# Performance work log

Measured on AMD Instinct MI355X. Metric: run time of the kernel, lower is better.

## Reference

```python
import jax, jax.numpy as jnp
import numpy as np

B, N0, N1, FD, L, H = 4, 256, 256, 128, 3, 1
NG = N0 + N1            # nodes per graph
N = B * NG              # total nodes
EPS_BN = 1e-5
EPS_SM = 1e-16


def _build_edges():
    def perm_edges(n, off):
        idx = np.arange(n)
        a = np.repeat(idx, n); b = np.tile(idx, n)
        m = a != b
        return np.stack([a[m], b[m]]) + off
    e_intra = np.concatenate([perm_edges(N0, 0), perm_edges(N1, N0)], axis=1)
    a = np.arange(N0); b = np.arange(N0, N0 + N1)
    cross1 = np.stack([np.repeat(a, N1), np.tile(b, N0)])
    cross2 = np.stack([np.repeat(b, N0), np.tile(a, N1)])
    eg = np.concatenate([e_intra, cross1, cross2], axis=1)
    tg = np.concatenate([np.zeros(e_intra.shape[1], np.int32),
                         np.ones(cross1.shape[1] + cross2.shape[1], np.int32)])
    ei = np.concatenate([eg + g * NG for g in range(B)], axis=1).astype(np.int32)
    et = np.tile(tg, B).astype(np.int32)
    return jnp.asarray(ei), jnp.asarray(et)


def setup_inputs() -> dict:
    key = jax.random.key(0)
    ks = jax.random.split(key, 8)
    edge_index, edge_type = _build_edges()
    return {
        'desc0': jax.random.normal(ks[0], (B, FD, N0), jnp.float32),
        'desc1': jax.random.normal(ks[1], (B, FD, N1), jnp.float32),
        'W': jax.random.normal(ks[2], (L, 2, FD, H * FD), jnp.float32) * (1.0 / np.sqrt(FD)),
        'q': jax.random.normal(ks[3], (L, H * FD, H), jnp.float32) * 0.1,
        'k': jax.random.normal(ks[4], (L, H * FD, H), jnp.float32) * 0.1,
        'conv_b': jnp.zeros((L, FD), jnp.float32),
        'lin_W': jax.random.normal(ks[5], (L, FD, 2 * FD), jnp.float32) * (1.0 / np.sqrt(2 * FD)),
        'lin_b': jnp.zeros((L, FD), jnp.float32),
        'gamma': jnp.ones((L, FD), jnp.float32),
        'beta': jnp.zeros((L, FD), jnp.float32),
        'edge_index': edge_index,
        'edge_type': edge_type,
    }


def _forward(desc0, desc1, W, q, k, conv_b, lin_W, lin_b, gamma, beta, edge_index, edge_type):
    # x: [B, NG, FD] -> flattened batch graph [N, FD]
    x = jnp.concatenate([desc0, desc1], axis=2)        # [B, FD, NG]
    x = jnp.transpose(x, (0, 2, 1)).reshape(N, FD)
    src, dst = edge_index[0], edge_index[1]
    nlayers = W.shape[0]
    heads = q.shape[2]
    for l in range(nlayers):
        # relation-specific node projections (equiv to per-edge bmm with weight[edge_type])
        proj = jnp.einsum('nf,rfo->nro', x, W[l])       # [N, 2, H*FD]
        out_i = proj[dst, edge_type]                    # [E, H*FD]
        out_j = proj[src, edge_type]                    # [E, H*FD]
        alpha = jax.nn.leaky_relu(out_i @ q[l] + out_j @ k[l], 0.2)  # [E, H]
        # softmax over incoming edges of each destination node (across-relation)
        amax = jax.ops.segment_max(alpha, dst, num_segments=N)
        ex = jnp.exp(alpha - amax[dst])
        denom = jax.ops.segment_sum(ex, dst, num_segments=N)
        att = ex / (denom[dst] + EPS_SM)                # [E, H]
        msg = (att[:, :, None] * out_j.reshape(-1, heads, FD)).reshape(-1, heads * FD)
        agg = jax.ops.segment_sum(msg, dst, num_segments=N).reshape(N, heads, FD)
        m1 = jax.nn.relu(agg.mean(axis=1) + conv_b[l])  # concat=False -> mean over heads
        m2 = jnp.concatenate([x, m1], axis=1) @ lin_W[l].T + lin_b[l]
        mu = m2.mean(axis=0)
        var = ((m2 - mu) ** 2).mean(axis=0)             # biased var (BatchNorm training)
        m3 = (m2 - mu) / jnp.sqrt(var + EPS_BN) * gamma[l] + beta[l]
        x = x + m3
    x = x.reshape(B, NG, FD).transpose(0, 2, 1)         # [B, FD, NG]
    return x


def reference(desc0, desc1, W, q, k, conv_b, lin_W, lin_b, gamma, beta, edge_index, edge_type):
    x = _forward(desc0, desc1, W, q, k, conv_b, lin_W, lin_b, gamma, beta, edge_index, edge_type)
    return x[:, :, :N0], x[:, :, N0:]
```

## Files before the change

### kernel.cpp

```cpp
#include <hip/hip_runtime.h>

#define FD  128
#define NN  2048

#define OFF_X     0
#define OFF_PROJ  262144
#define OFF_QS    786432
#define OFF_KS    790528
#define OFF_SUMS  794624
#define OFF_LWT   800768
#define OFF_M2    899072

__device__ __forceinline__ int swizzle_n0(int bid) {
    int g    = (bid & 7) >> 1;
    int slot = ((bid >> 3) << 1) | (bid & 1);
    return g*512 + slot*4;
}

__device__ __forceinline__ void proj_qsks4(
    const float* __restrict__ W, const float* __restrict__ qv,
    const float* __restrict__ kv, float* __restrict__ ws,
    int l, int n0, int t, const float (*xs)[FD],
    float (*redp)[256], float* red)
{
    int kh = t >> 8, tp = t & 255;
    int rsel = tp >> 7, o = tp & 127;
    const float* Wl = W + ((size_t)(l*2 + rsel)*FD)*FD + o;
    float acc[4];
#pragma unroll
    for (int r = 0; r < 4; r++) acc[r] = 0.f;
    int kbase = kh * 64;
#pragma unroll
    for (int kk = 0; kk < 64; kk += 4) {
        int k4 = kbase + kk;
        float w0 = Wl[(k4+0)*FD], w1 = Wl[(k4+1)*FD];
        float w2 = Wl[(k4+2)*FD], w3 = Wl[(k4+3)*FD];
#pragma unroll
        for (int r = 0; r < 4; r++) {
            float4 xq = *(const float4*)&xs[r][k4];
            acc[r] += xq.x*w0 + xq.y*w1 + xq.z*w2 + xq.w*w3;
        }
    }
    if (kh == 1) {
#pragma unroll
        for (int r = 0; r < 4; r++) redp[r][tp] = acc[r];
    }
    __syncthreads();
    if (t < 256) {
#pragma unroll
        for (int r = 0; r < 4; r++) acc[r] += redp[r][tp];
#pragma unroll
        for (int r = 0; r < 4; r++)
            ws[OFF_PROJ + (size_t)(n0 + r)*256 + tp] = acc[r];

        float qq = qv[l*FD + o], kq = kv[l*FD + o];
        int lane = t & 63, w = t >> 6;
#pragma unroll
        for (int r = 0; r < 4; r++) {
            float vq = acc[r]*qq, vk = acc[r]*kq;
            for (int off = 32; off; off >>= 1) {
                vq += __shfl_xor(vq, off, 64);
                vk += __shfl_xor(vk, off, 64);
            }
            if (lane == 0) { red[w*8 + r*2] = vq; red[w*8 + r*2 + 1] = vk; }
        }
    }
    __syncthreads();
    if (t < 16) {
        int r = t & 3, rs = (t >> 2) & 1, wh = t >> 3;
        float v = red[(rs*2)*8 + r*2 + wh] + red[(rs*2 + 1)*8 + r*2 + wh];
        if (wh == 0) ws[OFF_QS + rs*NN + n0 + r] = v;
        else         ws[OFF_KS + rs*NN + n0 + r] = v;
    }
}

__global__ __launch_bounds__(512, 4) void k_pre(
    const float* __restrict__ d0, const float* __restrict__ d1,
    const float* __restrict__ W,  const float* __restrict__ qv,
    const float* __restrict__ kv, const float* __restrict__ linW,
    float* __restrict__ ws)
{
    int bid = blockIdx.x, t = threadIdx.x;
    if (bid >= 512) {
        if (bid < 536) {
            int vb = bid - 512;
#pragma unroll
            for (int i = 0; i < 8; i++) {
                int e = vb*4096 + i*512 + t;
                int l = e >> 15, rem = e & 32767;
                int o = rem >> 8, c = rem & 255;
                ws[OFF_LWT + l*32768 + c*FD + o] = linW[e];
            }
        } else {
            for (int i = t; i < 6144; i += 512) ws[OFF_SUMS + i] = 0.f;
        }
        return;
    }
    __shared__ __attribute__((aligned(16))) float xs[4][FD];
    __shared__ float redp[4][256];
    __shared__ float red[32];
    int n0 = swizzle_n0(bid);
    {
        int row = t >> 7, f = t & 127;
        int n = n0 + row, gg = n >> 9, ii = n & 511;
        float v = (ii < 256) ? d0[gg*32768 + f*256 + ii]
                             : d1[gg*32768 + f*256 + (ii - 256)];
        xs[row][f] = v;
        ws[OFF_X + (size_t)n*FD + f] = v;
    }
    __syncthreads();
    proj_qsks4(W, qv, kv, ws, 0, n0, t, xs, redp, red);
}

__global__ __launch_bounds__(512, 4) void k_bp(
    const float* __restrict__ W,     const float* __restrict__ qv,
    const float* __restrict__ kv,    const float* __restrict__ gamma,
    const float* __restrict__ beta,  float* __restrict__ ws, int l)
{
    __shared__ float scale[FD], shift[FD];
    __shared__ __attribute__((aligned(16))) float xs[4][FD];
    __shared__ float redp[4][256];
    __shared__ float red[32];
    int bid = blockIdx.x, t = threadIdx.x;
    int lp = l - 1;
    if (t < 128) {
        float s0 = 0.f, s1 = 0.f;
#pragma unroll
        for (int sl = 0; sl < 8; sl++) {
            s0 += ws[OFF_SUMS + lp*2048 + sl*256 + t];
            s1 += ws[OFF_SUMS + lp*2048 + sl*256 + 128 + t];
        }
        float mu  = s0 * (1.f/2048.f);
        float var = s1 * (1.f/2048.f) - mu*mu;
        float rs  = rsqrtf(var + 1e-5f);
        float gm  = gamma[lp*FD + t], bt = beta[lp*FD + t];
        scale[t] = gm * rs;
        shift[t] = bt - mu * gm * rs;
    }
    __syncthreads();
    int n0 = swizzle_n0(bid);
    {
        int row = t >> 7, f = t & 127;
        size_t e = (size_t)(n0 + row)*FD + f;
        float xv = ws[OFF_X + e] + ws[OFF_M2 + e]*scale[f] + shift[f];
        xs[row][f] = xv;
        ws[OFF_X + e] = xv;
    }
    __syncthreads();
    proj_qsks4(W, qv, kv, ws, l, n0, t, xs, redp, red);
}

__global__ __launch_bounds__(512, 4) void k_attn(
    const float* __restrict__ convb, const float* __restrict__ linb,
    float* __restrict__ ws, int l)
{
    __shared__ __attribute__((aligned(16))) float att[4*512];
    __shared__ __attribute__((aligned(16))) float redB[8*4*128];
    __shared__ __attribute__((aligned(16))) float cat[4*256];
    __shared__ float sml[4][2], sls[4][2];
    __shared__ float r1[FD], r2[FD];

    int bid = blockIdx.x, t = threadIdx.x;
    int dstbase = swizzle_n0(bid);
    int g = dstbase >> 9, dloc0 = dstbase & 511;
    int Gd = (dloc0 >= 256) ? 1 : 0;

    {
        int w = t >> 6, p = t & 63;
        int d = w >> 1, h = w & 1;
        int dloc = dloc0 + d;
        float q0 = ws[OFF_QS + dstbase + d];
        float q1 = ws[OFF_QS + NN + dstbase + d];
        float sc[4];
#pragma unroll
        for (int j = 0; j < 4; j++) {
            int s = h*256 + p + j*64;
            int ts = (s < 256) ? Gd : 1 - Gd;
            float a = (ts ? q1 : q0) + ws[OFF_KS + ts*NN + g*512 + s];
            a = a > 0.f ? a : 0.2f*a;
            sc[j] = (s == dloc) ? -1e30f : a;
        }
        float lm = fmaxf(fmaxf(sc[0], sc[1]), fmaxf(sc[2], sc[3]));
        for (int off = 32; off; off >>= 1) lm = fmaxf(lm, __shfl_xor(lm, off, 64));
        float ex[4], lsum = 0.f;
#pragma unroll
        for (int j = 0; j < 4; j++) { ex[j] = __expf(sc[j] - lm); lsum += ex[j]; }
        for (int off = 32; off; off >>= 1) lsum += __shfl_xor(lsum, off, 64);
#pragma unroll
        for (int j = 0; j < 4; j++) att[d*512 + h*256 + p + j*64] = ex[j];
        if (p == 0) { sml[d][h] = lm; sls[d][h] = lsum; }
    }
    __syncthreads();
    {
        int d = t >> 7, s4 = (t & 127) * 4;
        int h = (s4 >= 256) ? 1 : 0;
        float m0 = sml[d][0], m1 = sml[d][1];
        float M = fmaxf(m0, m1);
        float denom = sls[d][0]*__expf(m0 - M) + sls[d][1]*__expf(m1 - M) + 1e-16f;
        float fac = __expf(sml[d][h] - M) / denom;
        float4 a4 = *(float4*)&att[d*512 + s4];
        a4.x *= fac; a4.y *= fac; a4.z *= fac; a4.w *= fac;
        *(float4*)&att[d*512 + s4] = a4;
        if (t < 128) r1[t] = 0.f;
        else if (t < 256) r2[t - 128] = 0.f;
    }
    __syncthreads();

    int f4 = t & 31, sq = t >> 5;
    float acc[4][4];
#pragma unroll
    for (int d2 = 0; d2 < 4; d2++)
#pragma unroll
        for (int j = 0; j < 4; j++) acc[d2][j] = 0.f;
    {
        int ts = (sq < 8) ? Gd : 1 - Gd;
        const float* P = ws + OFF_PROJ + (size_t)(g*512)*256 + ts*128 + f4*4;
        int s0 = sq * 32;
        float4 bufA[4], bufB[4];
#pragma unroll
        for (int u = 0; u < 4; u++) bufA[u] = *(const float4*)&P[(size_t)(s0+u)*256];
#pragma unroll
        for (int ii = 0; ii < 8; ii++) {
            const float4* cur = (ii & 1) ? bufB : bufA;
            float4*       nxt = (ii & 1) ? bufA : bufB;
            if (ii < 7) {
#pragma unroll
                for (int u = 0; u < 4; u++)
                    nxt[u] = *(const float4*)&P[(size_t)(s0 + (ii+1)*4 + u)*256];
            }
#pragma unroll
            for (int u = 0; u < 4; u++) {
                int s = s0 + ii*4 + u;
                float4 p4 = cur[u];
#pragma unroll
                for (int d2 = 0; d2 < 4; d2++) {
                    float b = att[d2*512 + s];
                    acc[d2][0] += b*p4.x; acc[d2][1] += b*p4.y;
                    acc[d2][2] += b*p4.z; acc[d2][3] += b*p4.w;
                }
            }
        }
    }
    if (sq >= 8) {
#pragma unroll
        for (int d2 = 0; d2 < 4; d2++)
            *(float4*)&redB[((sq - 8)*4 + d2)*128 + f4*4] =
                make_float4(acc[d2][0], acc[d2][1], acc[d2][2], acc[d2][3]);
    }
    __syncthreads();
    if (sq < 8) {
#pragma unroll
        for (int d2 = 0; d2 < 4; d2++) {
            float4 p4 = *(const float4*)&redB[(sq*4 + d2)*128 + f4*4];
            *(float4*)&redB[(sq*4 + d2)*128 + f4*4] =
                make_float4(acc[d2][0]+p4.x, acc[d2][1]+p4.y, acc[d2][2]+p4.z, acc[d2][3]+p4.w);
        }
    }
    __syncthreads();

    {
        int d2 = t >> 7, f = t & 127;
        float agg = 0.f;
#pragma unroll
        for (int cc = 0; cc < 8; cc++) agg += redB[(cc*4 + d2)*128 + f];
        float m1v = fmaxf(agg + convb[l*FD + f], 0.f);
        cat[d2*256 + FD + f] = m1v;
        cat[d2*256 + f] = ws[OFF_X + (size_t)(dstbase + d2)*FD + f];
    }
    __syncthreads();

#pragma unroll
    for (int d2 = 0; d2 < 4; d2++)
#pragma unroll
        for (int j = 0; j < 4; j++) acc[d2][j] = 0.f;
    {
        const float* lwt = ws + OFF_LWT + l*32768 + f4*4;
        int c0 = sq * 16;
        float4 bufA[4], bufB[4];
#pragma unroll
        for (int u = 0; u < 4; u++) bufA[u] = *(const float4*)&lwt[(c0+u)*128];
#pragma unroll
        for (int ii = 0; ii < 4; ii++) {
            const float4* cur = (ii & 1) ? bufB : bufA;
            float4*       nxt = (ii & 1) ? bufA : bufB;
            if (ii < 3) {
#pragma unroll
                for (int u = 0; u < 4; u++)
                    nxt[u] = *(const float4*)&lwt[(c0 + (ii+1)*4 + u)*128];
            }
#pragma unroll
            for (int u = 0; u < 4; u++) {
                int c = c0 + ii*4 + u;
                float4 w4 = cur[u];
#pragma unroll
                for (int d2 = 0; d2 < 4; d2++) {
                    float cv = cat[d2*256 + c];
                    acc[d2][0] += cv*w4.x; acc[d2][1] += cv*w4.y;
                    acc[d2][2] += cv*w4.z; acc[d2][3] += cv*w4.w;
                }
            }
        }
    }
    if (sq >= 8) {
#pragma unroll
        for (int d2 = 0; d2 < 4; d2++)
            *(float4*)&redB[((sq - 8)*4 + d2)*128 + f4*4] =
                make_float4(acc[d2][0], acc[d2][1], acc[d2][2], acc[d2][3]);
    }
    __syncthreads();
    if (sq < 8) {
#pragma unroll
        for (int d2 = 0; d2 < 4; d2++) {
            float4 p4 = *(const float4*)&redB[(sq*4 + d2)*128 + f4*4];
            *(float4*)&redB[(sq*4 + d2)*128 + f4*4] =
                make_float4(acc[d2][0]+p4.x, acc[d2][1]+p4.y, acc[d2][2]+p4.z, acc[d2][3]+p4.w);
        }
    }
    __syncthreads();

    {
        int d2 = t >> 7, o = t & 127;
        float m2v = linb[l*FD + o];
#pragma unroll
        for (int cc = 0; cc < 8; cc++) m2v += redB[(cc*4 + d2)*128 + o];
        ws[OFF_M2 + (size_t)(dstbase + d2)*FD + o] = m2v;
        atomicAdd(&r1[o], m2v);
        atomicAdd(&r2[o], m2v*m2v);
    }
    __syncthreads();
    if (t < 128) {
        int slot = bid & 7;
        atomicAdd(&ws[OFF_SUMS + l*2048 + slot*256 + t],       r1[t]);
        atomicAdd(&ws[OFF_SUMS + l*2048 + slot*256 + 128 + t], r2[t]);
    }
}

__global__ __launch_bounds__(256) void k_bnout(
    const float* __restrict__ gamma, const float* __restrict__ beta,
    float* __restrict__ ws, float* __restrict__ out)
{
    __shared__ float scale[FD], shift[FD];
    int bid = blockIdx.x, t = threadIdx.x;
    if (t < 128) {
        float s0 = 0.f, s1 = 0.f;
#pragma unroll
        for (int sl = 0; sl < 8; sl++) {
            s0 += ws[OFF_SUMS + 2*2048 + sl*256 + t];
            s1 += ws[OFF_SUMS + 2*2048 + sl*256 + 128 + t];
        }
        float mu  = s0 * (1.f/2048.f);
        float var = s1 * (1.f/2048.f) - mu*mu;
        float rs  = rsqrtf(var + 1e-5f);
        float gm  = gamma[2*FD + t], bt = beta[2*FD + t];
        scale[t] = gm * rs;
        shift[t] = bt - mu * gm * rs;
    }
    __syncthreads();
#pragma unroll
    for (int i = 0; i < 2; i++) {
        int idx = bid*512 + i*256 + t;
        int f = idx & 127, n = idx >> 7;
        float v = ws[OFF_X + idx] + ws[OFF_M2 + idx]*scale[f] + shift[f];
        int gg = n >> 9, ii = n & 511;
        int off = (ii < 256) ? (gg*32768 + f*256 + ii)
                             : (131072 + gg*32768 + f*256 + (ii - 256));
        out[off] = v;
    }
}

extern "C" void kernel_launch(void* const* d_in, const int* in_sizes, int n_in,
                              void* d_out, int out_size, void* d_ws, size_t ws_size,
                              hipStream_t stream) {
    (void)in_sizes; (void)n_in; (void)out_size; (void)ws_size;
    const float* desc0 = (const float*)d_in[0];
    const float* desc1 = (const float*)d_in[1];
    const float* W     = (const float*)d_in[2];
    const float* q     = (const float*)d_in[3];
    const float* kk    = (const float*)d_in[4];
    const float* convb = (const float*)d_in[5];
    const float* linW  = (const float*)d_in[6];
    const float* linb  = (const float*)d_in[7];
    const float* gamma = (const float*)d_in[8];
    const float* beta  = (const float*)d_in[9];
    float* ws  = (float*)d_ws;
    float* out = (float*)d_out;

    hipLaunchKernelGGL(k_pre,  dim3(537), dim3(512), 0, stream, desc0, desc1, W, q, kk, linW, ws);
    hipLaunchKernelGGL(k_attn, dim3(512), dim3(512), 0, stream, convb, linb, ws, 0);
    hipLaunchKernelGGL(k_bp,   dim3(512), dim3(512), 0, stream, W, q, kk, gamma, beta, ws, 1);
    hipLaunchKernelGGL(k_attn, dim3(512), dim3(512), 0, stream, convb, linb, ws, 1);
    hipLaunchKernelGGL(k_bp,   dim3(512), dim3(512), 0, stream, W, q, kk, gamma, beta, ws, 2);
    hipLaunchKernelGGL(k_attn, dim3(512), dim3(512), 0, stream, convb, linb, ws, 2);
    hipLaunchKernelGGL(k_bnout, dim3(512), dim3(256), 0, stream, gamma, beta, ws, out);
}
```

Measured before the change: 156.2 us.

## Aggregate raw node features before projection and precompute W·q, W·k vectors

Removes the per-node relation projection buffer. Attention now aggregates raw x over source nodes per relation, and the relation weight W is applied afterwards to the aggregated features, which works because the projection is linear. Query and key scalars come from precomputed W·q and W·k vectors, so the per-layer projection kernel becomes a cheap dot-product kernel. This avoids writing and reading the 2048x256 projection tensor every layer. In exchange, each attention block does an extra small GEMM reading W from global memory and needs an extra reduction stage.

Result: slower. 170.8 us (+9.4%).

```diff
diff --git a/kernel.cpp b/kernel.cpp
--- a/kernel.cpp
+++ b/kernel.cpp
@@ -4,12 +4,13 @@
 #define NN  2048
 
 #define OFF_X     0
-#define OFF_PROJ  262144
-#define OFF_QS    786432
-#define OFF_KS    790528
-#define OFF_SUMS  794624
-#define OFF_LWT   800768
-#define OFF_M2    899072
+#define OFF_QS    262144
+#define OFF_KS    266240
+#define OFF_SUMS  270336
+#define OFF_LWT   276480
+#define OFF_M2    374784
+#define OFF_QH    636928
+#define OFF_KH    637696
 
 __device__ __forceinline__ int swizzle_n0(int bid) {
     int g    = (bid & 7) >> 1;
@@ -17,15 +18,15 @@
     return g*512 + slot*4;
 }
 
-__device__ __forceinline__ void proj_qsks4(
+__device__ __forceinline__ void qsks0(
     const float* __restrict__ W, const float* __restrict__ qv,
     const float* __restrict__ kv, float* __restrict__ ws,
-    int l, int n0, int t, const float (*xs)[FD],
+    int n0, int t, const float (*xs)[FD],
     float (*redp)[256], float* red)
 {
     int kh = t >> 8, tp = t & 255;
     int rsel = tp >> 7, o = tp & 127;
-    const float* Wl = W + ((size_t)(l*2 + rsel)*FD)*FD + o;
+    const float* Wl = W + ((size_t)rsel*FD)*FD + o;
     float acc[4];
 #pragma unroll
     for (int r = 0; r < 4; r++) acc[r] = 0.f;
@@ -49,11 +50,7 @@
     if (t < 256) {
 #pragma unroll
         for (int r = 0; r < 4; r++) acc[r] += redp[r][tp];
-#pragma unroll
-        for (int r = 0; r < 4; r++)
-            ws[OFF_PROJ + (size_t)(n0 + r)*256 + tp] = acc[r];
-
-        float qq = qv[l*FD + o], kq = kv[l*FD + o];
+        float qq = qv[o], kq = kv[o];
         int lane = t & 63, w = t >> 6;
 #pragma unroll
         for (int r = 0; r < 4; r++) {
@@ -93,6 +90,17 @@
             }
         } else {
             for (int i = t; i < 6144; i += 512) ws[OFF_SUMS + i] = 0.f;
+#pragma unroll
+            for (int ii = 0; ii < 3; ii++) {
+                int e = ii*512 + t;
+                int sel = e & 1, idx = e >> 1;
+                const float* wrow = W + (size_t)idx*FD;
+                int l = idx >> 8;
+                const float* vvec = sel ? (kv + l*FD) : (qv + l*FD);
+                float acc = 0.f;
+                for (int o = 0; o < FD; o++) acc += wrow[o]*vvec[o];
+                ws[(sel ? OFF_KH : OFF_QH) + idx] = acc;
+            }
         }
         return;
     }
@@ -109,18 +117,15 @@
         ws[OFF_X + (size_t)n*FD + f] = v;
     }
     __syncthreads();
-    proj_qsks4(W, qv, kv, ws, 0, n0, t, xs, redp, red);
-}
-
-__global__ __launch_bounds__(512, 4) void k_bp(
-    const float* __restrict__ W,     const float* __restrict__ qv,
-    const float* __restrict__ kv,    const float* __restrict__ gamma,
-    const float* __restrict__ beta,  float* __restrict__ ws, int l)
+    qsks0(W, qv, kv, ws, n0, t, xs, redp, red);
+}
+
+__global__ __launch_bounds__(512, 4) void k_qs(
+    const float* __restrict__ gamma, const float* __restrict__ beta,
+    float* __restrict__ ws, int l)
 {
     __shared__ float scale[FD], shift[FD];
-    __shared__ __attribute__((aligned(16))) float xs[4][FD];
-    __shared__ float redp[4][256];
-    __shared__ float red[32];
+    __shared__ float red[4][8];
     int bid = blockIdx.x, t = threadIdx.x;
     int lp = l - 1;
     if (t < 128) {
@@ -139,24 +144,44 @@
     }
     __syncthreads();
     int n0 = swizzle_n0(bid);
-    {
-        int row = t >> 7, f = t & 127;
-        size_t e = (size_t)(n0 + row)*FD + f;
-        float xv = ws[OFF_X + e] + ws[OFF_M2 + e]*scale[f] + shift[f];
-        xs[row][f] = xv;
-        ws[OFF_X + e] = xv;
-    }
-    __syncthreads();
-    proj_qsks4(W, qv, kv, ws, l, n0, t, xs, redp, red);
+    int row = t >> 7, f = t & 127;
+    size_t e = (size_t)(n0 + row)*FD + f;
+    float xv = ws[OFF_X + e] + ws[OFF_M2 + e]*scale[f] + shift[f];
+    ws[OFF_X + e] = xv;
+    float p0 = xv * ws[OFF_QH + l*256 + f];
+    float p1 = xv * ws[OFF_QH + l*256 + 128 + f];
+    float p2 = xv * ws[OFF_KH + l*256 + f];
+    float p3 = xv * ws[OFF_KH + l*256 + 128 + f];
+    for (int off = 32; off; off >>= 1) {
+        p0 += __shfl_xor(p0, off, 64);
+        p1 += __shfl_xor(p1, off, 64);
+        p2 += __shfl_xor(p2, off, 64);
+        p3 += __shfl_xor(p3, off, 64);
+    }
+    int lane = t & 63, wh = (t >> 6) & 1;
+    if (lane == 0) {
+        red[row][wh*4+0] = p0; red[row][wh*4+1] = p1;
+        red[row][wh*4+2] = p2; red[row][wh*4+3] = p3;
+    }
+    __syncthreads();
+    if (t < 16) {
+        int r = t >> 2, j = t & 3;
+        float v = red[r][j] + red[r][4+j];
+        int n = n0 + r;
+        if      (j == 0) ws[OFF_QS + n] = v;
+        else if (j == 1) ws[OFF_QS + NN + n] = v;
+        else if (j == 2) ws[OFF_KS + n] = v;
+        else             ws[OFF_KS + NN + n] = v;
+    }
 }
 
 __global__ __launch_bounds__(512, 4) void k_attn(
-    const float* __restrict__ convb, const float* __restrict__ linb,
-    float* __restrict__ ws, int l)
+    const float* __restrict__ Wg,    const float* __restrict__ convb,
+    const float* __restrict__ linb,  float* __restrict__ ws, int l)
 {
     __shared__ __attribute__((aligned(16))) float att[4*512];
     __shared__ __attribute__((aligned(16))) float redB[8*4*128];
-    __shared__ __attribute__((aligned(16))) float cat[4*256];
+    __shared__ __attribute__((aligned(16))) float hgc[4*256];
     __shared__ float sml[4][2], sls[4][2];
     __shared__ float r1[FD], r2[FD];
 
@@ -213,12 +238,11 @@
 #pragma unroll
         for (int j = 0; j < 4; j++) acc[d2][j] = 0.f;
     {
-        int ts = (sq < 8) ? Gd : 1 - Gd;
-        const float* P = ws + OFF_PROJ + (size_t)(g*512)*256 + ts*128 + f4*4;
+        const float* xp = ws + OFF_X + (size_t)(g*512)*FD + f4*4;
         int s0 = sq * 32;
         float4 bufA[4], bufB[4];
 #pragma unroll
-        for (int u = 0; u < 4; u++) bufA[u] = *(const float4*)&P[(size_t)(s0+u)*256];
+        for (int u = 0; u < 4; u++) bufA[u] = *(const float4*)&xp[(size_t)(s0+u)*FD];
 #pragma unroll
         for (int ii = 0; ii < 8; ii++) {
             const float4* cur = (ii & 1) ? bufB : bufA;
@@ -226,17 +250,80 @@
             if (ii < 7) {
 #pragma unroll
                 for (int u = 0; u < 4; u++)
-                    nxt[u] = *(const float4*)&P[(size_t)(s0 + (ii+1)*4 + u)*256];
+                    nxt[u] = *(const float4*)&xp[(size_t)(s0 + (ii+1)*4 + u)*FD];
             }
 #pragma unroll
             for (int u = 0; u < 4; u++) {
                 int s = s0 + ii*4 + u;
-                float4 p4 = cur[u];
+                float4 v = cur[u];
 #pragma unroll
                 for (int d2 = 0; d2 < 4; d2++) {
                     float b = att[d2*512 + s];
-                    acc[d2][0] += b*p4.x; acc[d2][1] += b*p4.y;
-                    acc[d2][2] += b*p4.z; acc[d2][3] += b*p4.w;
+                    acc[d2][0] += b*v.x; acc[d2][1] += b*v.y;
+                    acc[d2][2] += b*v.z; acc[d2][3] += b*v.w;
+                }
+            }
+        }
+    }
+    {
+        int slot = (sq & 3) + ((sq >> 3) << 2);
+        if (sq & 4) {
+#pragma unroll
+            for (int d2 = 0; d2 < 4; d2++)
+                *(float4*)&redB[(slot*4 + d2)*128 + f4*4] =
+                    make_float4(acc[d2][0], acc[d2][1], acc[d2][2], acc[d2][3]);
+        }
+        __syncthreads();
+        if (!(sq & 4)) {
+#pragma unroll
+            for (int d2 = 0; d2 < 4; d2++) {
+                float4 p4 = *(const float4*)&redB[(slot*4 + d2)*128 + f4*4];
+                *(float4*)&redB[(slot*4 + d2)*128 + f4*4] =
+                    make_float4(acc[d2][0]+p4.x, acc[d2][1]+p4.y, acc[d2][2]+p4.z, acc[d2][3]+p4.w);
+            }
+        }
+        __syncthreads();
+    }
+    {
+        int d2 = t >> 7, f = t & 127;
+        float hg0 = redB[(0*4+d2)*128+f] + redB[(1*4+d2)*128+f]
+                  + redB[(2*4+d2)*128+f] + redB[(3*4+d2)*128+f];
+        float hg1 = redB[(4*4+d2)*128+f] + redB[(5*4+d2)*128+f]
+                  + redB[(6*4+d2)*128+f] + redB[(7*4+d2)*128+f];
+        hgc[d2*256 + f]       = Gd ? hg1 : hg0;
+        hgc[d2*256 + 128 + f] = Gd ? hg0 : hg1;
+    }
+    __syncthreads();
+
+#pragma unroll
+    for (int d2 = 0; d2 < 4; d2++)
+#pragma unroll
+        for (int j = 0; j < 4; j++) acc[d2][j] = 0.f;
+    {
+        int rel = sq >> 3;
+        const float* wp = Wg + ((size_t)((l*2 + rel)*FD) + (sq & 7)*16)*FD + f4*4;
+        int c0 = sq * 16;
+        float4 wA[4], wB[4];
+#pragma unroll
+        for (int u = 0; u < 4; u++) wA[u] = *(const float4*)&wp[(size_t)u*FD];
+#pragma unroll
+        for (int ii = 0; ii < 4; ii++) {
+            const float4* cur = (ii & 1) ? wB : wA;
+            float4*       nxt = (ii & 1) ? wA : wB;
+            if (ii < 3) {
+#pragma unroll
+                for (int u = 0; u < 4; u++)
+                    nxt[u] = *(const float4*)&wp[(size_t)((ii+1)*4 + u)*FD];
+            }
+#pragma unroll
+            for (int u = 0; u < 4; u++) {
+                int c = c0 + ii*4 + u;
+                float4 w4 = cur[u];
+#pragma unroll
+                for (int d2 = 0; d2 < 4; d2++) {
+                    float cv = hgc[d2*256 + c];
+                    acc[d2][0] += cv*w4.x; acc[d2][1] += cv*w4.y;
+                    acc[d2][2] += cv*w4.z; acc[d2][3] += cv*w4.w;
                 }
             }
         }
@@ -264,8 +351,8 @@
 #pragma unroll
         for (int cc = 0; cc < 8; cc++) agg += redB[(cc*4 + d2)*128 + f];
         float m1v = fmaxf(agg + convb[l*FD + f], 0.f);
-        cat[d2*256 + FD + f] = m1v;
-        cat[d2*256 + f] = ws[OFF_X + (size_t)(dstbase + d2)*FD + f];
+        hgc[d2*256 + 128 + f] = m1v;
+        hgc[d2*256 + f] = ws[OFF_X + (size_t)(dstbase + d2)*FD + f];
     }
     __syncthreads();
 
@@ -276,13 +363,13 @@
     {
         const float* lwt = ws + OFF_LWT + l*32768 + f4*4;
         int c0 = sq * 16;
-        float4 bufA[4], bufB[4];
-#pragma unroll
-        for (int u = 0; u < 4; u++) bufA[u] = *(const float4*)&lwt[(c0+u)*128];
+        float4 wA[4], wB[4];
+#pragma unroll
+        for (int u = 0; u < 4; u++) wA[u] = *(const float4*)&lwt[(c0+u)*128];
 #pragma unroll
         for (int ii = 0; ii < 4; ii++) {
-            const float4* cur = (ii & 1) ? bufB : bufA;
-            float4*       nxt = (ii & 1) ? bufA : bufB;
+            const float4* cur = (ii & 1) ? wB : wA;
+            float4*       nxt = (ii & 1) ? wA : wB;
             if (ii < 3) {
 #pragma unroll
                 for (int u = 0; u < 4; u++)
@@ -294,7 +381,7 @@
                 float4 w4 = cur[u];
 #pragma unroll
                 for (int d2 = 0; d2 < 4; d2++) {
-                    float cv = cat[d2*256 + c];
+                    float cv = hgc[d2*256 + c];
                     acc[d2][0] += cv*w4.x; acc[d2][1] += cv*w4.y;
                     acc[d2][2] += cv*w4.z; acc[d2][3] += cv*w4.w;
                 }
@@ -386,10 +473,10 @@
     float* out = (float*)d_out;
 
     hipLaunchKernelGGL(k_pre,  dim3(537), dim3(512), 0, stream, desc0, desc1, W, q, kk, linW, ws);
-    hipLaunchKernelGGL(k_attn, dim3(512), dim3(512), 0, stream, convb, linb, ws, 0);
-    hipLaunchKernelGGL(k_bp,   dim3(512), dim3(512), 0, stream, W, q, kk, gamma, beta, ws, 1);
-    hipLaunchKernelGGL(k_attn, dim3(512), dim3(512), 0, stream, convb, linb, ws, 1);
-    hipLaunchKernelGGL(k_bp,   dim3(512), dim3(512), 0, stream, W, q, kk, gamma, beta, ws, 2);
-    hipLaunchKernelGGL(k_attn, dim3(512), dim3(512), 0, stream, convb, linb, ws, 2);
+    hipLaunchKernelGGL(k_attn, dim3(512), dim3(512), 0, stream, W, convb, linb, ws, 0);
+    hipLaunchKernelGGL(k_qs,   dim3(512), dim3(512), 0, stream, gamma, beta, ws, 1);
+    hipLaunchKernelGGL(k_attn, dim3(512), dim3(512), 0, stream, W, convb, linb, ws, 1);
+    hipLaunchKernelGGL(k_qs,   dim3(512), dim3(512), 0, stream, gamma, beta, ws, 2);
+    hipLaunchKernelGGL(k_attn, dim3(512), dim3(512), 0, stream, W, convb, linb, ws, 2);
     hipLaunchKernelGGL(k_bnout, dim3(512), dim3(256), 0, stream, gamma, beta, ws, out);
 }
```
